# Optimization experiments

Measured on AMD Instinct MI355X. Metric: run time of the kernel, lower is better.

The kernel has to match this reference:

```python
import jax, jax.numpy as jnp
import numpy as np

BS = 2
EMBED = 256
NH = 8
NL = 4
NP = 4
HD = EMBED // NH
SHAPES = [(128, 128), (64, 64), (32, 32), (16, 16)]
NQ = sum(h * w for h, w in SHAPES)  # 21760


def setup_inputs() -> dict:
    key = jax.random.key(0)
    ks = jax.random.split(key, 12)
    s = 1.0 / np.sqrt(EMBED)
    return {
        "query": jax.random.normal(ks[0], (BS, NQ, EMBED), jnp.float32),
        "reference_points": jax.random.uniform(ks[1], (BS, NQ, NL, 2), jnp.float32),
        "value": jax.random.normal(ks[2], (BS, NQ, EMBED), jnp.float32),
        "W_off": jax.random.normal(ks[3], (EMBED, NH * NL * NP * 2), jnp.float32) * 0.01,
        "b_off": jax.random.normal(ks[4], (NH * NL * NP * 2,), jnp.float32) * 0.5,
        "W_attn": jax.random.normal(ks[5], (EMBED, NH * NL * NP), jnp.float32) * 0.02,
        "b_attn": jnp.zeros((NH * NL * NP,), jnp.float32),
        "W_v": jax.random.normal(ks[6], (EMBED, EMBED), jnp.float32) * s,
        "b_v": jnp.zeros((EMBED,), jnp.float32),
        "W_out": jax.random.normal(ks[7], (EMBED, EMBED), jnp.float32) * s,
        "b_out": jnp.zeros((EMBED,), jnp.float32),
        "value_spatial_shapes": np.asarray(SHAPES, dtype=np.int64),
    }


def _ms_deform_attn(value, shapes, loc, aw):
    # value: [bs,V,nh,d]; loc: [bs,nq,nh,L,P,2] in [0,1]; aw: [bs,nq,nh,L,P]
    bs, V, nh, d = value.shape
    nq = loc.shape[1]
    out = jnp.zeros((bs, nq, nh, d), value.dtype)
    start = 0
    b_idx = jnp.arange(bs)[:, None, None, None]
    h_idx = jnp.arange(nh)[None, None, :, None]
    for l, (H, W) in enumerate(shapes):
        H, W = int(H), int(W)
        v = value[:, start:start + H * W].reshape(bs, H, W, nh, d)
        start += H * W
        g = 2.0 * loc[:, :, :, l] - 1.0  # [bs,nq,nh,P,2], grid_sample convention
        # align_corners=False pixel coordinates
        x = ((g[..., 0] + 1.0) * W - 1.0) * 0.5
        y = ((g[..., 1] + 1.0) * H - 1.0) * 0.5
        x0 = jnp.floor(x); y0 = jnp.floor(y)
        wx1 = x - x0; wx0 = 1.0 - wx1
        wy1 = y - y0; wy0 = 1.0 - wy1

        def gather(yi, xi):
            inb = (yi >= 0) & (yi < H) & (xi >= 0) & (xi < W)
            yc = jnp.clip(yi, 0, H - 1).astype(jnp.int32)
            xc = jnp.clip(xi, 0, W - 1).astype(jnp.int32)
            vals = v[b_idx, yc, xc, h_idx]  # [bs,nq,nh,P,d]
            return vals * inb[..., None].astype(v.dtype)

        samp = (gather(y0, x0) * (wy0 * wx0)[..., None]
                + gather(y0, x0 + 1) * (wy0 * wx1)[..., None]
                + gather(y0 + 1, x0) * (wy1 * wx0)[..., None]
                + gather(y0 + 1, x0 + 1) * (wy1 * wx1)[..., None])
        out = out + jnp.einsum('bqhpd,bqhp->bqhd', samp, aw[:, :, :, l])
    return out.reshape(bs, nq, nh * d)


def reference(query, reference_points, value, W_off, b_off, W_attn, b_attn,
              W_v, b_v, W_out, b_out, value_spatial_shapes):
    shapes = np.asarray(value_spatial_shapes)  # static [L,2]
    bs, nq, _ = query.shape
    v = (value @ W_v + b_v).reshape(bs, -1, NH, HD)
    off = (query @ W_off + b_off).reshape(bs, nq, NH, NL, NP, 2)
    aw = (query @ W_attn + b_attn).reshape(bs, nq, NH, NL * NP)
    aw = jax.nn.softmax(aw, axis=-1).reshape(bs, nq, NH, NL, NP)
    # offset normalizer: (W,H) per level
    norm = jnp.asarray(shapes[:, ::-1].astype(np.float32))  # [L,2]
    loc = reference_points[:, :, None, :, None, :] + off / norm[None, None, None, :, None, :]
    out = _ms_deform_attn(v, shapes, loc, aw)
    return out @ W_out + b_out
```

## Files before the change

kernel.cpp:

```cpp
#include <hip/hip_runtime.h>
#include <math.h>

#define BS 2
#define NQ 21760
#define V_LEN 21760
#define EMBED 256
#define NH 8
#define NL 4
#define NP 4
#define HD 32

typedef _Float16 f16;
typedef _Float16 half8 __attribute__((ext_vector_type(8)));
typedef _Float16 half4v __attribute__((ext_vector_type(4)));
typedef float f32x4 __attribute__((ext_vector_type(4)));

__device__ __forceinline__ void load_lds16(const void* g, void* l) {
    __builtin_amdgcn_global_load_lds(
        (const __attribute__((address_space(1))) void*)g,
        (__attribute__((address_space(3))) void*)l, 16, 0, 0);
}

__global__ __launch_bounds__(256) void prep(
    const float* __restrict__ W_v, const float* __restrict__ W_off,
    const float* __restrict__ W_attn, const float* __restrict__ W_out,
    const float* __restrict__ b_off, const float* __restrict__ b_attn,
    f16* __restrict__ WTv, f16* __restrict__ WToa, f16* __restrict__ WTu,
    float* __restrict__ bcat)
{
    const int nb = blockIdx.x;
    const int k = threadIdx.x;
    if (nb < 256) {
        WTv[nb * 256 + k] = (f16)W_v[k * 256 + nb];
    } else if (nb < 640) {
        int j = nb - 256;
        float w = (j < 256) ? W_off[k * 256 + j] : W_attn[k * 128 + (j - 256)];
        WToa[j * 256 + k] = (f16)w;
    } else if (nb < 896) {
        int j = nb - 640;
        WTu[j * 256 + k] = (f16)W_out[k * 256 + j];
    } else if (nb == 896) {
        bcat[k] = b_off[k];
        if (k < 128) bcat[256 + k] = b_attn[k];
    }
}

template<bool AF16, bool OUTF16>
__global__ __launch_bounds__(256) void gemm_mfma(
    const void* __restrict__ Av, const f16* __restrict__ WT,
    const float* __restrict__ bias, void* __restrict__ Cv,
    int N, int ntn)
{
    const int bnt = blockIdx.x % ntn;
    const int bmt = blockIdx.x / ntn;
    const int bm = bmt * 64, bn = bnt * 128;
    const int K = 256;

    __shared__ __align__(16) f16 As[4 * 64 * 8];
    __shared__ __align__(16) f16 Bs[4 * 128 * 8];

    const int tid = threadIdx.x;
    const int lane = tid & 63, wv = tid >> 6;
    const int quad = lane >> 4, l16 = lane & 15;

    f32x4 acc[4][2];
    #pragma unroll
    for (int i = 0; i < 4; i++)
        #pragma unroll
        for (int j = 0; j < 2; j++)
            acc[i][j] = (f32x4){0.f, 0.f, 0.f, 0.f};

    for (int k0 = 0; k0 < K; k0 += 32) {
        #pragma unroll
        for (int i = 0; i < 2; i++) {
            int S0 = (i * 4 + wv) * 64;
            int S = S0 + lane;
            int col = S & 127, kcg = S >> 7;
            load_lds16(&WT[(size_t)(bn + col) * K + k0 + kcg * 8], &Bs[S0 * 8]);
        }
        if constexpr (AF16) {
            const f16* A = (const f16*)Av;
            int S0 = wv * 64;
            int S = S0 + lane;
            int row = S & 63, kcg = S >> 6;
            load_lds16(&A[(size_t)(bm + row) * K + k0 + kcg * 8], &As[S0 * 8]);
        } else {
            const float* A = (const float*)Av;
            #pragma unroll
            for (int i = 0; i < 2; i++) {
                int F = i * 256 + tid;
                int row = F >> 3, kq = F & 7;
                float4 f = *(const float4*)&A[(size_t)(bm + row) * K + k0 + kq * 4];
                half4v h;
                h[0] = (f16)f.x; h[1] = (f16)f.y; h[2] = (f16)f.z; h[3] = (f16)f.w;
                *(half4v*)&As[((kq >> 1) * 64 + row) * 8 + (kq & 1) * 4] = h;
            }
        }
        __syncthreads();

        half8 af[4], bf[2];
        #pragma unroll
        for (int mi = 0; mi < 4; mi++)
            af[mi] = *(const half8*)&As[(quad * 64 + mi * 16 + l16) * 8];
        #pragma unroll
        for (int ni = 0; ni < 2; ni++)
            bf[ni] = *(const half8*)&Bs[(quad * 128 + wv * 32 + ni * 16 + l16) * 8];
        #pragma unroll
        for (int mi = 0; mi < 4; mi++)
            #pragma unroll
            for (int ni = 0; ni < 2; ni++)
                acc[mi][ni] = __builtin_amdgcn_mfma_f32_16x16x32_f16(
                    af[mi], bf[ni], acc[mi][ni], 0, 0, 0);
        __syncthreads();
    }

    #pragma unroll
    for (int mi = 0; mi < 4; mi++) {
        #pragma unroll
        for (int ni = 0; ni < 2; ni++) {
            const int col = bn + wv * 32 + ni * 16 + l16;
            const int row0 = bm + mi * 16 + quad * 4;
            const float bc = bias[col];
            #pragma unroll
            for (int r = 0; r < 4; r++) {
                float v = acc[mi][ni][r] + bc;
                if constexpr (OUTF16)
                    ((f16*)Cv)[(size_t)(row0 + r) * N + col] = (f16)v;
                else
                    ((float*)Cv)[(size_t)(row0 + r) * N + col] = v;
            }
        }
    }
}

__global__ __launch_bounds__(256) void deform_sample(
    const f16* __restrict__ vproj, const float* __restrict__ offaw,
    const float* __restrict__ refp, f16* __restrict__ sampled)
{
    const int wv = threadIdx.x >> 6;
    const int lane = threadIdx.x & 63;
    const int q = blockIdx.x * 4 + wv;
    const int b = blockIdx.y;
    const int bq = b * NQ + q;

    __shared__ float s_off[4][256];
    __shared__ float s_aw[4][128];
    __shared__ __align__(16) float s_w[4][128][4];
    __shared__ __align__(16) int   s_idx[4][128][4];

    const float* row = offaw + (size_t)bq * 384;
    #pragma unroll
    for (int i = 0; i < 4; i++) s_off[wv][lane + i * 64] = row[lane + i * 64];
    #pragma unroll
    for (int i = 0; i < 2; i++) s_aw[wv][lane + i * 64] = row[256 + lane + i * 64];
    __syncthreads();

    if (lane < 8) {
        float m = -1e30f;
        #pragma unroll
        for (int i = 0; i < 16; i++) m = fmaxf(m, s_aw[wv][lane * 16 + i]);
        float ssum = 0.f;
        #pragma unroll
        for (int i = 0; i < 16; i++) {
            float e = __expf(s_aw[wv][lane * 16 + i] - m);
            s_aw[wv][lane * 16 + i] = e;
            ssum += e;
        }
        float r = 1.0f / ssum;
        #pragma unroll
        for (int i = 0; i < 16; i++) s_aw[wv][lane * 16 + i] *= r;
    }
    __syncthreads();

    #pragma unroll
    for (int sI = 0; sI < 2; sI++) {
        int d = lane + sI * 64;
        int h = d & 7, lp = d >> 3, l = lp >> 2, p = lp & 3;
        int Wl = 128 >> l;
        int st = (l == 0) ? 0 : (l == 1) ? 16384 : (l == 2) ? 20480 : 21504;
        float rx = refp[(size_t)bq * 8 + l * 2 + 0];
        float ry = refp[(size_t)bq * 8 + l * 2 + 1];
        float ox = s_off[wv][((h * NL + l) * NP + p) * 2 + 0];
        float oy = s_off[wv][((h * NL + l) * NP + p) * 2 + 1];
        float fW = (float)Wl;
        float x = (rx + ox / fW) * fW - 0.5f;
        float y = (ry + oy / fW) * fW - 0.5f;
        float xf = floorf(x), yf = floorf(y);
        int x0 = (int)xf, y0 = (int)yf;
        float wx1 = x - xf, wx0 = 1.f - wx1;
        float wy1 = y - yf, wy0 = 1.f - wy1;
        float aw = s_aw[wv][h * 16 + lp];
        bool vx0 = (x0 >= 0) && (x0 < Wl);
        bool vx1 = (x0 + 1 >= 0) && (x0 + 1 < Wl);
        bool vy0 = (y0 >= 0) && (y0 < Wl);
        bool vy1 = (y0 + 1 >= 0) && (y0 + 1 < Wl);
        int cx0 = min(max(x0, 0), Wl - 1), cx1 = min(max(x0 + 1, 0), Wl - 1);
        int cy0 = min(max(y0, 0), Wl - 1), cy1 = min(max(y0 + 1, 0), Wl - 1);
        s_idx[wv][d][0] = (st + cy0 * Wl + cx0) << 9;  s_w[wv][d][0] = (vy0 && vx0) ? wy0 * wx0 * aw : 0.f;
        s_idx[wv][d][1] = (st + cy0 * Wl + cx1) << 9;  s_w[wv][d][1] = (vy0 && vx1) ? wy0 * wx1 * aw : 0.f;
        s_idx[wv][d][2] = (st + cy1 * Wl + cx0) << 9;  s_w[wv][d][2] = (vy1 && vx0) ? wy1 * wx0 * aw : 0.f;
        s_idx[wv][d][3] = (st + cy1 * Wl + cx1) << 9;  s_w[wv][d][3] = (vy1 && vx1) ? wy1 * wx1 * aw : 0.f;
    }
    __syncthreads();

    const int h = lane >> 3;
    const unsigned int cb = (unsigned int)lane * 8u;
    const char* vb = (const char*)(vproj + (size_t)b * V_LEN * EMBED);
    float a0 = 0.f, a1 = 0.f, a2 = 0.f, a3 = 0.f;
    #pragma unroll 4
    for (int lp = 0; lp < 16; lp++) {
        const int d = lp * 8 + h;
        const float4 w4 = *(const float4*)&s_w[wv][d][0];
        const int4  i4 = *(const int4*)&s_idx[wv][d][0];
        half4v v0 = *(const half4v*)(vb + ((unsigned int)i4.x + cb));
        half4v v1 = *(const half4v*)(vb + ((unsigned int)i4.y + cb));
        half4v v2 = *(const half4v*)(vb + ((unsigned int)i4.z + cb));
        half4v v3 = *(const half4v*)(vb + ((unsigned int)i4.w + cb));
        a0 += w4.x * (float)v0[0] + w4.y * (float)v1[0] + w4.z * (float)v2[0] + w4.w * (float)v3[0];
        a1 += w4.x * (float)v0[1] + w4.y * (float)v1[1] + w4.z * (float)v2[1] + w4.w * (float)v3[1];
        a2 += w4.x * (float)v0[2] + w4.y * (float)v1[2] + w4.z * (float)v2[2] + w4.w * (float)v3[2];
        a3 += w4.x * (float)v0[3] + w4.y * (float)v1[3] + w4.z * (float)v2[3] + w4.w * (float)v3[3];
    }

    half4v o;
    o[0] = (f16)a0; o[1] = (f16)a1; o[2] = (f16)a2; o[3] = (f16)a3;
    *(half4v*)&sampled[(size_t)bq * 256 + lane * 4] = o;
}

extern "C" void kernel_launch(void* const* d_in, const int* in_sizes, int n_in,
                              void* d_out, int out_size, void* d_ws, size_t ws_size,
                              hipStream_t stream)
{
    const float* query  = (const float*)d_in[0];
    const float* refp   = (const float*)d_in[1];
    const float* value  = (const float*)d_in[2];
    const float* W_off  = (const float*)d_in[3];
    const float* b_off  = (const float*)d_in[4];
    const float* W_attn = (const float*)d_in[5];
    const float* b_attn = (const float*)d_in[6];
    const float* W_v    = (const float*)d_in[7];
    const float* b_v    = (const float*)d_in[8];
    const float* W_out  = (const float*)d_in[9];
    const float* b_out  = (const float*)d_in[10];
    float* out = (float*)d_out;

    const int M = BS * NQ;

    char* ws = (char*)d_ws;
    f16*   WTv   = (f16*)ws;    ws += 256 * 256 * 2;
    f16*   WToa  = (f16*)ws;    ws += 384 * 256 * 2;
    f16*   WTu   = (f16*)ws;    ws += 256 * 256 * 2;
    float* bcat  = (float*)ws;  ws += 384 * 4 + 128;
    f16*   vproj = (f16*)ws;    ws += (size_t)M * 256 * 2;
    float* offaw = (float*)ws;  ws += (size_t)M * 384 * 4;
    f16*   samp  = (f16*)ws;    ws += (size_t)M * 256 * 2;

    prep<<<897, 256, 0, stream>>>(W_v, W_off, W_attn, W_out, b_off, b_attn,
                                  WTv, WToa, WTu, bcat);
    gemm_mfma<false, true><<<(M / 64) * 2, 256, 0, stream>>>(value, WTv, b_v, vproj, 256, 2);
    gemm_mfma<false, false><<<(M / 64) * 3, 256, 0, stream>>>(query, WToa, bcat, offaw, 384, 3);
    deform_sample<<<dim3(NQ / 4, BS), 256, 0, stream>>>(vproj, offaw, refp, samp);
    gemm_mfma<true, false><<<(M / 64) * 2, 256, 0, stream>>>(samp, WTu, b_out, out, 256, 2);
}
```

Before: 331.0 us.

## Enlarge GEMM tiles to 128x128, merge front GEMMs, store fp16 sampling weights

```diff
diff --git a/kernel.cpp b/kernel.cpp
--- a/kernel.cpp
+++ b/kernel.cpp
@@ -45,29 +45,26 @@
     }
 }
 
-template<bool AF16, bool OUTF16>
-__global__ __launch_bounds__(256) void gemm_mfma(
+template<bool AF16>
+__device__ __forceinline__ void gemm128_core(
     const void* __restrict__ Av, const f16* __restrict__ WT,
     const float* __restrict__ bias, void* __restrict__ Cv,
-    int N, int ntn)
-{
-    const int bnt = blockIdx.x % ntn;
-    const int bmt = blockIdx.x / ntn;
-    const int bm = bmt * 64, bn = bnt * 128;
+    int N, int bm, int bn, bool outF16)
+{
     const int K = 256;
-
-    __shared__ __align__(16) f16 As[4 * 64 * 8];
+    __shared__ __align__(16) f16 As[4 * 128 * 8];
     __shared__ __align__(16) f16 Bs[4 * 128 * 8];
 
     const int tid = threadIdx.x;
     const int lane = tid & 63, wv = tid >> 6;
+    const int wr = wv >> 1, wc = wv & 1;
     const int quad = lane >> 4, l16 = lane & 15;
 
-    f32x4 acc[4][2];
+    f32x4 acc[4][4];
     #pragma unroll
     for (int i = 0; i < 4; i++)
         #pragma unroll
-        for (int j = 0; j < 2; j++)
+        for (int j = 0; j < 4; j++)
             acc[i][j] = (f32x4){0.f, 0.f, 0.f, 0.f};
 
     for (int k0 = 0; k0 < K; k0 += 32) {
@@ -80,35 +77,38 @@
         }
         if constexpr (AF16) {
             const f16* A = (const f16*)Av;
-            int S0 = wv * 64;
-            int S = S0 + lane;
-            int row = S & 63, kcg = S >> 6;
-            load_lds16(&A[(size_t)(bm + row) * K + k0 + kcg * 8], &As[S0 * 8]);
+            #pragma unroll
+            for (int i = 0; i < 2; i++) {
+                int S0 = (i * 4 + wv) * 64;
+                int S = S0 + lane;
+                int row = S & 127, kcg = S >> 7;
+                load_lds16(&A[(size_t)(bm + row) * K + k0 + kcg * 8], &As[S0 * 8]);
+            }
         } else {
             const float* A = (const float*)Av;
             #pragma unroll
-            for (int i = 0; i < 2; i++) {
+            for (int i = 0; i < 4; i++) {
                 int F = i * 256 + tid;
                 int row = F >> 3, kq = F & 7;
                 float4 f = *(const float4*)&A[(size_t)(bm + row) * K + k0 + kq * 4];
                 half4v h;
                 h[0] = (f16)f.x; h[1] = (f16)f.y; h[2] = (f16)f.z; h[3] = (f16)f.w;
-                *(half4v*)&As[((kq >> 1) * 64 + row) * 8 + (kq & 1) * 4] = h;
+                *(half4v*)&As[((kq >> 1) * 128 + row) * 8 + (kq & 1) * 4] = h;
             }
         }
         __syncthreads();
 
-        half8 af[4], bf[2];
+        half8 af[4], bf[4];
         #pragma unroll
         for (int mi = 0; mi < 4; mi++)
-            af[mi] = *(const half8*)&As[(quad * 64 + mi * 16 + l16) * 8];
-        #pragma unroll
-        for (int ni = 0; ni < 2; ni++)
-            bf[ni] = *(const half8*)&Bs[(quad * 128 + wv * 32 + ni * 16 + l16) * 8];
+            af[mi] = *(const half8*)&As[(quad * 128 + wr * 64 + mi * 16 + l16) * 8];
+        #pragma unroll
+        for (int ni = 0; ni < 4; ni++)
+            bf[ni] = *(const half8*)&Bs[(quad * 128 + wc * 64 + ni * 16 + l16) * 8];
         #pragma unroll
         for (int mi = 0; mi < 4; mi++)
             #pragma unroll
-            for (int ni = 0; ni < 2; ni++)
+            for (int ni = 0; ni < 4; ni++)
                 acc[mi][ni] = __builtin_amdgcn_mfma_f32_16x16x32_f16(
                     af[mi], bf[ni], acc[mi][ni], 0, 0, 0);
         __syncthreads();
@@ -117,20 +117,46 @@
     #pragma unroll
     for (int mi = 0; mi < 4; mi++) {
         #pragma unroll
-        for (int ni = 0; ni < 2; ni++) {
-            const int col = bn + wv * 32 + ni * 16 + l16;
-            const int row0 = bm + mi * 16 + quad * 4;
+        for (int ni = 0; ni < 4; ni++) {
+            const int col = bn + wc * 64 + ni * 16 + l16;
+            const int row0 = bm + wr * 64 + mi * 16 + quad * 4;
             const float bc = bias[col];
-            #pragma unroll
-            for (int r = 0; r < 4; r++) {
-                float v = acc[mi][ni][r] + bc;
-                if constexpr (OUTF16)
-                    ((f16*)Cv)[(size_t)(row0 + r) * N + col] = (f16)v;
-                else
-                    ((float*)Cv)[(size_t)(row0 + r) * N + col] = v;
+            if (outF16) {
+                #pragma unroll
+                for (int r = 0; r < 4; r++)
+                    ((f16*)Cv)[(size_t)(row0 + r) * N + col] = (f16)(acc[mi][ni][r] + bc);
+            } else {
+                #pragma unroll
+                for (int r = 0; r < 4; r++)
+                    ((float*)Cv)[(size_t)(row0 + r) * N + col] = acc[mi][ni][r] + bc;
             }
         }
     }
+}
+
+__global__ __launch_bounds__(256) void front_gemm(
+    const float* __restrict__ value, const float* __restrict__ query,
+    const f16* __restrict__ WTv, const f16* __restrict__ WToa,
+    const float* __restrict__ b_v, const float* __restrict__ bcat,
+    f16* __restrict__ vproj, float* __restrict__ offaw)
+{
+    int bid = blockIdx.x;
+    if (bid < 680) {
+        int bnt = bid & 1, bmt = bid >> 1;
+        gemm128_core<false>(value, WTv, b_v, vproj, 256, bmt * 128, bnt * 128, true);
+    } else {
+        int b2 = bid - 680;
+        int bnt = b2 % 3, bmt = b2 / 3;
+        gemm128_core<false>(query, WToa, bcat, offaw, 384, bmt * 128, bnt * 128, false);
+    }
+}
+
+__global__ __launch_bounds__(256) void out_gemm(
+    const f16* __restrict__ samp, const f16* __restrict__ WTu,
+    const float* __restrict__ b_out, float* __restrict__ out)
+{
+    int bnt = blockIdx.x & 1, bmt = blockIdx.x >> 1;
+    gemm128_core<true>(samp, WTu, b_out, out, 256, bmt * 128, bnt * 128, false);
 }
 
 __global__ __launch_bounds__(256) void deform_sample(
@@ -145,8 +171,8 @@
 
     __shared__ float s_off[4][256];
     __shared__ float s_aw[4][128];
-    __shared__ __align__(16) float s_w[4][128][4];
-    __shared__ __align__(16) int   s_idx[4][128][4];
+    __shared__ __align__(16) f16  s_w[4][128][4];
+    __shared__ __align__(16) int  s_idx[4][128][4];
 
     const float* row = offaw + (size_t)bq * 384;
     #pragma unroll
@@ -196,10 +222,18 @@
         bool vy1 = (y0 + 1 >= 0) && (y0 + 1 < Wl);
         int cx0 = min(max(x0, 0), Wl - 1), cx1 = min(max(x0 + 1, 0), Wl - 1);
         int cy0 = min(max(y0, 0), Wl - 1), cy1 = min(max(y0 + 1, 0), Wl - 1);
-        s_idx[wv][d][0] = (st + cy0 * Wl + cx0) << 9;  s_w[wv][d][0] = (vy0 && vx0) ? wy0 * wx0 * aw : 0.f;
-        s_idx[wv][d][1] = (st + cy0 * Wl + cx1) << 9;  s_w[wv][d][1] = (vy0 && vx1) ? wy0 * wx1 * aw : 0.f;
-        s_idx[wv][d][2] = (st + cy1 * Wl + cx0) << 9;  s_w[wv][d][2] = (vy1 && vx0) ? wy1 * wx0 * aw : 0.f;
-        s_idx[wv][d][3] = (st + cy1 * Wl + cx1) << 9;  s_w[wv][d][3] = (vy1 && vx1) ? wy1 * wx1 * aw : 0.f;
+        half4v w4;
+        w4[0] = (f16)((vy0 && vx0) ? wy0 * wx0 * aw : 0.f);
+        w4[1] = (f16)((vy0 && vx1) ? wy0 * wx1 * aw : 0.f);
+        w4[2] = (f16)((vy1 && vx0) ? wy1 * wx0 * aw : 0.f);
+        w4[3] = (f16)((vy1 && vx1) ? wy1 * wx1 * aw : 0.f);
+        *(half4v*)&s_w[wv][d][0] = w4;
+        int4 i4;
+        i4.x = (st + cy0 * Wl + cx0) << 9;
+        i4.y = (st + cy0 * Wl + cx1) << 9;
+        i4.z = (st + cy1 * Wl + cx0) << 9;
+        i4.w = (st + cy1 * Wl + cx1) << 9;
+        *(int4*)&s_idx[wv][d][0] = i4;
     }
     __syncthreads();
 
@@ -207,19 +241,19 @@
     const unsigned int cb = (unsigned int)lane * 8u;
     const char* vb = (const char*)(vproj + (size_t)b * V_LEN * EMBED);
     float a0 = 0.f, a1 = 0.f, a2 = 0.f, a3 = 0.f;
-    #pragma unroll 4
+    #pragma unroll 8
     for (int lp = 0; lp < 16; lp++) {
         const int d = lp * 8 + h;
-        const float4 w4 = *(const float4*)&s_w[wv][d][0];
+        const half4v w4 = *(const half4v*)&s_w[wv][d][0];
         const int4  i4 = *(const int4*)&s_idx[wv][d][0];
         half4v v0 = *(const half4v*)(vb + ((unsigned int)i4.x + cb));
         half4v v1 = *(const half4v*)(vb + ((unsigned int)i4.y + cb));
         half4v v2 = *(const half4v*)(vb + ((unsigned int)i4.z + cb));
         half4v v3 = *(const half4v*)(vb + ((unsigned int)i4.w + cb));
-        a0 += w4.x * (float)v0[0] + w4.y * (float)v1[0] + w4.z * (float)v2[0] + w4.w * (float)v3[0];
-        a1 += w4.x * (float)v0[1] + w4.y * (float)v1[1] + w4.z * (float)v2[1] + w4.w * (float)v3[1];
-        a2 += w4.x * (float)v0[2] + w4.y * (float)v1[2] + w4.z * (float)v2[2] + w4.w * (float)v3[2];
-        a3 += w4.x * (float)v0[3] + w4.y * (float)v1[3] + w4.z * (float)v2[3] + w4.w * (float)v3[3];
+        a0 += (float)w4[0] * (float)v0[0] + (float)w4[1] * (float)v1[0] + (float)w4[2] * (float)v2[0] + (float)w4[3] * (float)v3[0];
+        a1 += (float)w4[0] * (float)v0[1] + (float)w4[1] * (float)v1[1] + (float)w4[2] * (float)v2[1] + (float)w4[3] * (float)v3[1];
+        a2 += (float)w4[0] * (float)v0[2] + (float)w4[1] * (float)v1[2] + (float)w4[2] * (float)v2[2] + (float)w4[3] * (float)v3[2];
+        a3 += (float)w4[0] * (float)v0[3] + (float)w4[1] * (float)v1[3] + (float)w4[2] * (float)v2[3] + (float)w4[3] * (float)v3[3];
     }
 
     half4v o;
@@ -257,8 +291,8 @@
 
     prep<<<897, 256, 0, stream>>>(W_v, W_off, W_attn, W_out, b_off, b_attn,
                                   WTv, WToa, WTu, bcat);
-    gemm_mfma<false, true><<<(M / 64) * 2, 256, 0, stream>>>(value, WTv, b_v, vproj, 256, 2);
-    gemm_mfma<false, false><<<(M / 64) * 3, 256, 0, stream>>>(query, WToa, bcat, offaw, 384, 3);
+    front_gemm<<<1700, 256, 0, stream>>>(value, query, WTv, WToa, b_v, bcat,
+                                         vproj, offaw);
     deform_sample<<<dim3(NQ / 4, BS), 256, 0, stream>>>(vproj, offaw, refp, samp);
-    gemm_mfma<true, false><<<(M / 64) * 2, 256, 0, stream>>>(samp, WTu, b_out, out, 256, 2);
-}
+    out_gemm<<<680, 256, 0, stream>>>(samp, WTu, b_out, out);
+}
```

New measurement: 311.6 us. -5.9%, faster.
